# Optimization experiments

Measured on AMD Instinct MI355X. Metric: run time of the kernel, lower is better.

Reference implementation:

```python
import jax, jax.numpy as jnp
import numpy as np

S, B, IN, OUT = 32, 256, 1024, 1024

def setup_inputs() -> dict:
    key = jax.random.key(0)
    ks = jax.random.split(key, 7)
    return {
        "input": jax.random.normal(ks[0], (S, B, IN), dtype=jnp.float32),
        "weight_mu": jax.random.normal(ks[1], (OUT, IN), dtype=jnp.float32) * 0.1,
        "weight_rho": jax.random.normal(ks[2], (OUT, IN), dtype=jnp.float32) - 3.0,
        "bias_mu": jax.random.normal(ks[3], (OUT,), dtype=jnp.float32) * 0.1,
        "bias_rho": jax.random.normal(ks[4], (OUT,), dtype=jnp.float32) - 3.0,
        "eps_w": jax.random.normal(ks[5], (S, OUT, IN), dtype=jnp.float32),
        "eps_b": jax.random.normal(ks[6], (S, OUT), dtype=jnp.float32),
    }

def reference(input, weight_mu, weight_rho, bias_mu, bias_rho, eps_w, eps_b):
    # sigma = log(1 + exp(rho))  (softplus)
    weight_sigma = jax.nn.softplus(weight_rho)              # (out, in)
    bias_sigma = jax.nn.softplus(bias_rho)                  # (out,)
    # reparameterized samples: (S, out, in) and (S, out)
    weight = weight_mu[None, :, :] + weight_sigma[None, :, :] * eps_w
    bias = bias_mu[None, :] + bias_sigma[None, :] * eps_b
    # batch_linear: per-sample x @ W^T + b
    out = jnp.einsum('sbi,soi->sbo', input, weight) + bias[:, None, :]
    return out
```

## Files before the change

### kernel.cpp

```cpp
#include <hip/hip_runtime.h>
#include <hip/hip_bf16.h>

constexpr int kS   = 32;
constexpr int kB   = 256;
constexpr int kIN  = 1024;
constexpr int kOUT = 1024;
constexpr int BN   = 64;
constexpr int BK   = 32;
constexpr int NT   = kIN / BK;

typedef __bf16 v4bf __attribute__((ext_vector_type(4)));
typedef __bf16 v8bf __attribute__((ext_vector_type(8)));
typedef float  v4f  __attribute__((ext_vector_type(4)));

__device__ __forceinline__ float softplus_f(float x) {
    return fmaxf(x, 0.0f) + log1pf(expf(-fabsf(x)));
}
__device__ __forceinline__ unsigned int bfbits(float x) {
    __bf16 h = (__bf16)x;
    unsigned short u;
    __builtin_memcpy(&u, &h, 2);
    return (unsigned int)u;
}
__device__ __forceinline__ float asf(unsigned int u) {
    float f; __builtin_memcpy(&f, &u, 4); return f;
}

__global__ void sigma_pack(const float* __restrict__ mu, const float* __restrict__ rho,
                           uint4* __restrict__ ms) {
    int gid = blockIdx.x * blockDim.x + threadIdx.x;
    float4 m = reinterpret_cast<const float4*>(mu)[gid];
    float4 r = reinterpret_cast<const float4*>(rho)[gid];
    uint4 o;
    o.x = bfbits(m.x) | (bfbits(softplus_f(r.x)) << 16);
    o.y = bfbits(m.y) | (bfbits(softplus_f(r.y)) << 16);
    o.z = bfbits(m.z) | (bfbits(softplus_f(r.z)) << 16);
    o.w = bfbits(m.w) | (bfbits(softplus_f(r.w)) << 16);
    ms[gid] = o;
}

__global__ void xcast_kernel(const float* __restrict__ X, __bf16* __restrict__ Xb) {
    size_t i = ((size_t)blockIdx.x * blockDim.x + threadIdx.x) * 8;
    float4 a = *reinterpret_cast<const float4*>(X + i);
    float4 b = *reinterpret_cast<const float4*>(X + i + 4);
    v8bf r;
    r[0] = (__bf16)a.x; r[1] = (__bf16)a.y; r[2] = (__bf16)a.z; r[3] = (__bf16)a.w;
    r[4] = (__bf16)b.x; r[5] = (__bf16)b.y; r[6] = (__bf16)b.z; r[7] = (__bf16)b.w;
    *reinterpret_cast<v8bf*>(Xb + i) = r;
}

__global__ __launch_bounds__(256, 4) void wmat(
        const unsigned int* __restrict__ MS,
        const float* __restrict__ Ew,
        __bf16* __restrict__ Wp)
{
    const int bb  = blockIdx.x;
    const int s   = bb & 31;
    const int rr  = bb >> 5;
    const int ot  = rr >> 2;
    const int q   = rr & 3;
    const int tid = threadIdx.x;

    const float*        Eg = Ew + ((size_t)s * kOUT + ot * 64) * kIN;
    const unsigned int* Mg = MS + (size_t)(ot * 64) * kIN;
    char* Wt = (char*)(Wp + ((size_t)(s * 16 + ot) * NT) * 2048);

    #pragma unroll 4
    for (int i = tid; i < 16 * 256; i += 256) {
        int row = q * 16 + (i >> 8);
        int k   = (i & 255) * 4;
        float4 e = *reinterpret_cast<const float4*>(Eg + (size_t)row * kIN + k);
        uint4  p = *reinterpret_cast<const uint4*>(Mg + (size_t)row * kIN + k);
        v4bf w;
        w[0] = (__bf16)fmaf(asf(p.x & 0xffff0000u), e.x, asf(p.x << 16));
        w[1] = (__bf16)fmaf(asf(p.y & 0xffff0000u), e.y, asf(p.y << 16));
        w[2] = (__bf16)fmaf(asf(p.z & 0xffff0000u), e.z, asf(p.z << 16));
        w[3] = (__bf16)fmaf(asf(p.w & 0xffff0000u), e.w, asf(p.w << 16));
        int t    = k >> 5;
        int slot = ((k >> 3) & 3) ^ ((row >> 1) & 3);
        *reinterpret_cast<v4bf*>(Wt + t * 4096 + row * 64 + slot * 16 + (k & 7) * 2) = w;
    }
}

#define GLDS16(g, l) __builtin_amdgcn_global_load_lds(                      \
    (const __attribute__((address_space(1))) void*)(g),                     \
    (__attribute__((address_space(3))) void*)(l), 16, 0, 0)
#define GLDS4(g, l) __builtin_amdgcn_global_load_lds(                       \
    (const __attribute__((address_space(1))) void*)(g),                     \
    (__attribute__((address_space(3))) void*)(l), 4, 0, 0)

__global__ __launch_bounds__(512, 4) void dv_gemm(
        const __bf16* __restrict__ Xb,
        const __bf16* __restrict__ Wp,
        const float* __restrict__ Bmu,
        const float* __restrict__ Brho,
        const float* __restrict__ Eb,
        float* __restrict__ O)
{
    __shared__ __attribute__((aligned(16))) __bf16 Xs[3][kB * BK];
    __shared__ __attribute__((aligned(16))) __bf16 Ws[3][BN * BK];

    const int tid = threadIdx.x, bb = blockIdx.x;
    const int xcd = bb & 7;
    const int jj  = bb >> 3;
    const int s   = (xcd << 2) | (jj & 3);
    const int ot  = jj >> 2;
    const int o_base = ot * BN;

    const int lane = tid & 63, wv = tid >> 6;
    const int mwv = wv >> 1, nwv = wv & 1;
    const int lr = lane & 15, kg = lane >> 4;

    const __bf16* Xbase = Xb + (size_t)s * kB * kIN;
    const char*   Wbase = (const char*)(Wp + ((size_t)(s * 16 + ot) * NT) * 2048);

    const int xrow = wv * 32 + (lane >> 2);
    const int xq0  = ((lane & 3) - (xrow >> 2)) & 3;
    const int xq1  = ((lane & 3) - ((xrow + 16) >> 2)) & 3;

    auto STAGE = [&](int t, int bf) {
        GLDS16(Xbase + (size_t)xrow * kIN + t * BK + xq0 * 8,
               &Xs[bf][(wv * 32) * BK]);
        GLDS16(Xbase + (size_t)(xrow + 16) * kIN + t * BK + xq1 * 8,
               &Xs[bf][(wv * 32 + 16) * BK]);
        const char* wt = Wbase + t * 4096 + wv * 512;
        char*       wl = (char*)&Ws[bf][0] + wv * 512;
        GLDS4(wt + lane * 4,       wl);
        GLDS4(wt + 256 + lane * 4, wl + 256);
    };

    v4f acc[4][2] = {};

    STAGE(0, 0);
    STAGE(1, 1);

    for (int t = 0; t < NT; ++t) {
        const int bf = t % 3;

        if (t < NT - 1)
            asm volatile("s_waitcnt vmcnt(4) lgkmcnt(0)" ::: "memory");
        else
            asm volatile("s_waitcnt vmcnt(0) lgkmcnt(0)" ::: "memory");
        __builtin_amdgcn_s_barrier();

        if (t + 2 < NT) STAGE(t + 2, (t + 2) % 3);

        v8bf a[4];
        #pragma unroll
        for (int mf = 0; mf < 4; ++mf) {
            int row = mwv * 64 + mf * 16 + lr;
            int ql  = (kg + (row >> 2)) & 3;
            a[mf] = *reinterpret_cast<const v8bf*>(&Xs[bf][row * BK + ql * 8]);
        }
        v8bf b[2];
        #pragma unroll
        for (int nf = 0; nf < 2; ++nf) {
            int row  = nwv * 32 + nf * 16 + lr;
            int slot = kg ^ ((row >> 1) & 3);
            b[nf] = *reinterpret_cast<const v8bf*>(
                (const char*)&Ws[bf][0] + row * 64 + slot * 16);
        }

        #pragma unroll
        for (int mf = 0; mf < 4; ++mf)
            #pragma unroll
            for (int nf = 0; nf < 2; ++nf)
                acc[mf][nf] = __builtin_amdgcn_mfma_f32_16x16x32_bf16(
                    a[mf], b[nf], acc[mf][nf], 0, 0, 0);
    }

    float bias[2];
    #pragma unroll
    for (int nf = 0; nf < 2; ++nf) {
        int o = o_base + nwv * 32 + nf * 16 + lr;
        bias[nf] = fmaf(softplus_f(Brho[o]), Eb[(size_t)s * kOUT + o], Bmu[o]);
    }
    #pragma unroll
    for (int mf = 0; mf < 4; ++mf) {
        #pragma unroll
        for (int rr = 0; rr < 4; ++rr) {
            int mrow = mwv * 64 + mf * 16 + kg * 4 + rr;
            float* orow = O + ((size_t)s * kB + mrow) * kOUT + o_base + nwv * 32;
            #pragma unroll
            for (int nf = 0; nf < 2; ++nf)
                __builtin_nontemporal_store(acc[mf][nf][rr] + bias[nf],
                                            orow + nf * 16 + lr);
        }
    }
}

__global__ void dv_naive(const float* __restrict__ X, const float* __restrict__ Wmu,
                         const float* __restrict__ Wrho, const float* __restrict__ Bmu,
                         const float* __restrict__ Brho, const float* __restrict__ Ew,
                         const float* __restrict__ Eb, float* __restrict__ O) {
    size_t gid = (size_t)blockIdx.x * blockDim.x + threadIdx.x;
    int o = gid % kOUT;
    int b = (gid / kOUT) % kB;
    int s = gid / ((size_t)kOUT * kB);
    const float* x = X + ((size_t)s * kB + b) * kIN;
    const float* e = Ew + ((size_t)s * kOUT + o) * kIN;
    const float* wm = Wmu + (size_t)o * kIN;
    const float* wr = Wrho + (size_t)o * kIN;
    float acc = 0.f;
    for (int k = 0; k < kIN; ++k)
        acc += x[k] * fmaf(softplus_f(wr[k]), e[k], wm[k]);
    O[gid] = acc + fmaf(softplus_f(Brho[o]), Eb[(size_t)s * kOUT + o], Bmu[o]);
}

extern "C" void kernel_launch(void* const* d_in, const int* in_sizes, int n_in,
                              void* d_out, int out_size, void* d_ws, size_t ws_size,
                              hipStream_t stream) {
    const float* input = (const float*)d_in[0];
    const float* w_mu  = (const float*)d_in[1];
    const float* w_rho = (const float*)d_in[2];
    const float* b_mu  = (const float*)d_in[3];
    const float* b_rho = (const float*)d_in[4];
    const float* eps_w = (const float*)d_in[5];
    const float* eps_b = (const float*)d_in[6];
    float* out = (float*)d_out;

    const size_t ms_bytes  = (size_t)kOUT * kIN * 4;
    const size_t xbf_bytes = (size_t)kS * kB * kIN * sizeof(__bf16);
    const size_t wp_bytes  = (size_t)kS * kOUT * kIN * sizeof(__bf16);

    if (ws_size < ms_bytes + xbf_bytes + wp_bytes) {
        dv_naive<<<dim3((size_t)kS * kB * kOUT / 256), 256, 0, stream>>>(
            input, w_mu, w_rho, b_mu, b_rho, eps_w, eps_b, out);
        return;
    }

    unsigned int* ms = (unsigned int*)d_ws;
    __bf16* xbf = (__bf16*)((char*)d_ws + ms_bytes);
    __bf16* wp  = (__bf16*)((char*)d_ws + ms_bytes + xbf_bytes);

    sigma_pack<<<dim3((kOUT * kIN) / (256 * 4)), 256, 0, stream>>>(w_mu, w_rho, (uint4*)ms);
    xcast_kernel<<<dim3((size_t)kS * kB * kIN / (256 * 8)), 256, 0, stream>>>(input, xbf);
    wmat<<<dim3(2048), 256, 0, stream>>>(ms, eps_w, wp);
    dv_gemm<<<dim3(kS * (kOUT / BN)), 512, 0, stream>>>(xbf, wp, b_mu, b_rho, eps_b, out);
}
```

Before: 302.1 us.

## Fuse weight sampling into GEMM by staging eps_w and packed mu/sigma in LDS

Removes the separate wmat kernel and its bf16 weight buffer. The GEMM now streams fp32 eps_w chunks and packed mu/sigma rows into double-buffered LDS, then builds the bf16 B fragments in registers with an FMA just before the MFMAs. The output tile shrinks from 64 to 32 columns, with a new multi-stream waitcnt schedule. This avoids writing and re-reading the materialised weight tensor in HBM. The cost is that X is read twice as often, and the larger LDS footprint likely leaves only one block per CU, which weakens latency hiding.

```diff
diff --git a/kernel.cpp b/kernel.cpp
--- a/kernel.cpp
+++ b/kernel.cpp
@@ -5,11 +5,11 @@
 constexpr int kB   = 256;
 constexpr int kIN  = 1024;
 constexpr int kOUT = 1024;
-constexpr int BN   = 64;
+constexpr int BN   = 32;
 constexpr int BK   = 32;
+constexpr int CK   = 256;
 constexpr int NT   = kIN / BK;
 
-typedef __bf16 v4bf __attribute__((ext_vector_type(4)));
 typedef __bf16 v8bf __attribute__((ext_vector_type(8)));
 typedef float  v4f  __attribute__((ext_vector_type(4)));
 
@@ -49,56 +49,22 @@
     *reinterpret_cast<v8bf*>(Xb + i) = r;
 }
 
-__global__ __launch_bounds__(256, 4) void wmat(
-        const unsigned int* __restrict__ MS,
-        const float* __restrict__ Ew,
-        __bf16* __restrict__ Wp)
-{
-    const int bb  = blockIdx.x;
-    const int s   = bb & 31;
-    const int rr  = bb >> 5;
-    const int ot  = rr >> 2;
-    const int q   = rr & 3;
-    const int tid = threadIdx.x;
-
-    const float*        Eg = Ew + ((size_t)s * kOUT + ot * 64) * kIN;
-    const unsigned int* Mg = MS + (size_t)(ot * 64) * kIN;
-    char* Wt = (char*)(Wp + ((size_t)(s * 16 + ot) * NT) * 2048);
-
-    #pragma unroll 4
-    for (int i = tid; i < 16 * 256; i += 256) {
-        int row = q * 16 + (i >> 8);
-        int k   = (i & 255) * 4;
-        float4 e = *reinterpret_cast<const float4*>(Eg + (size_t)row * kIN + k);
-        uint4  p = *reinterpret_cast<const uint4*>(Mg + (size_t)row * kIN + k);
-        v4bf w;
-        w[0] = (__bf16)fmaf(asf(p.x & 0xffff0000u), e.x, asf(p.x << 16));
-        w[1] = (__bf16)fmaf(asf(p.y & 0xffff0000u), e.y, asf(p.y << 16));
-        w[2] = (__bf16)fmaf(asf(p.z & 0xffff0000u), e.z, asf(p.z << 16));
-        w[3] = (__bf16)fmaf(asf(p.w & 0xffff0000u), e.w, asf(p.w << 16));
-        int t    = k >> 5;
-        int slot = ((k >> 3) & 3) ^ ((row >> 1) & 3);
-        *reinterpret_cast<v4bf*>(Wt + t * 4096 + row * 64 + slot * 16 + (k & 7) * 2) = w;
-    }
-}
-
 #define GLDS16(g, l) __builtin_amdgcn_global_load_lds(                      \
     (const __attribute__((address_space(1))) void*)(g),                     \
     (__attribute__((address_space(3))) void*)(l), 16, 0, 0)
-#define GLDS4(g, l) __builtin_amdgcn_global_load_lds(                       \
-    (const __attribute__((address_space(1))) void*)(g),                     \
-    (__attribute__((address_space(3))) void*)(l), 4, 0, 0)
-
-__global__ __launch_bounds__(512, 4) void dv_gemm(
+
+__global__ __launch_bounds__(512, 2) void dv_main(
         const __bf16* __restrict__ Xb,
-        const __bf16* __restrict__ Wp,
+        const unsigned int* __restrict__ MS,
+        const float* __restrict__ Ew,
         const float* __restrict__ Bmu,
         const float* __restrict__ Brho,
         const float* __restrict__ Eb,
         float* __restrict__ O)
 {
-    __shared__ __attribute__((aligned(16))) __bf16 Xs[3][kB * BK];
-    __shared__ __attribute__((aligned(16))) __bf16 Ws[3][BN * BK];
+    __shared__ __attribute__((aligned(16))) float        Ep[2][BN * CK];
+    __shared__ __attribute__((aligned(16))) unsigned int Mp[2][BN * (CK/2)];
+    __shared__ __attribute__((aligned(16))) __bf16       Xs[3][kB * BK];
 
     const int tid = threadIdx.x, bb = blockIdx.x;
     const int xcd = bb & 7;
@@ -108,61 +74,96 @@
     const int o_base = ot * BN;
 
     const int lane = tid & 63, wv = tid >> 6;
-    const int mwv = wv >> 1, nwv = wv & 1;
     const int lr = lane & 15, kg = lane >> 4;
 
     const __bf16* Xbase = Xb + (size_t)s * kB * kIN;
-    const char*   Wbase = (const char*)(Wp + ((size_t)(s * 16 + ot) * NT) * 2048);
-
     const int xrow = wv * 32 + (lane >> 2);
     const int xq0  = ((lane & 3) - (xrow >> 2)) & 3;
     const int xq1  = ((lane & 3) - ((xrow + 16) >> 2)) & 3;
 
-    auto STAGE = [&](int t, int bf) {
+    auto STAGE_X = [&](int t, int bf) {
         GLDS16(Xbase + (size_t)xrow * kIN + t * BK + xq0 * 8,
                &Xs[bf][(wv * 32) * BK]);
         GLDS16(Xbase + (size_t)(xrow + 16) * kIN + t * BK + xq1 * 8,
                &Xs[bf][(wv * 32 + 16) * BK]);
-        const char* wt = Wbase + t * 4096 + wv * 512;
-        char*       wl = (char*)&Ws[bf][0] + wv * 512;
-        GLDS4(wt + lane * 4,       wl);
-        GLDS4(wt + 256 + lane * 4, wl + 256);
     };
-
-    v4f acc[4][2] = {};
-
-    STAGE(0, 0);
-    STAGE(1, 1);
-
-    for (int t = 0; t < NT; ++t) {
-        const int bf = t % 3;
-
-        if (t < NT - 1)
+    auto STAGE_E = [&](int c, int bf) {
+        #pragma unroll
+        for (int j = 0; j < 4; ++j) {
+            int r = wv * 4 + j;
+            GLDS16(Ew + ((size_t)s * kOUT + o_base + r) * kIN + c * CK
+                       + ((lane ^ (r & 7)) << 2),
+                   (char*)&Ep[bf][0] + r * 1024);
+        }
+    };
+    auto STAGE_M = [&](int sub, int bf) {
+        #pragma unroll
+        for (int j = 0; j < 2; ++j) {
+            int r0 = j * 16 + wv * 2;
+            int r  = r0 + (lane >> 5);
+            GLDS16(MS + (size_t)(o_base + r) * kIN + sub * 128
+                      + (((lane & 31) ^ (r & 7)) << 2),
+                   (char*)&Mp[bf][0] + r0 * 512);
+        }
+    };
+
+    v4f acc[2][2] = {};
+
+    STAGE_E(0, 0);
+    STAGE_M(0, 0);
+    STAGE_X(0, 0);
+    STAGE_X(1, 1);
+
+    #pragma unroll
+    for (int T = 0; T < NT; ++T) {
+        if (T == 1 || T == 9 || T == 17)
+            asm volatile("s_waitcnt vmcnt(8) lgkmcnt(0)" ::: "memory");
+        else if (T == 5 || T == 13 || T == 21 || T == 25)
             asm volatile("s_waitcnt vmcnt(4) lgkmcnt(0)" ::: "memory");
+        else if (T == 31)
+            asm volatile("s_waitcnt vmcnt(0) lgkmcnt(0)" ::: "memory");
         else
-            asm volatile("s_waitcnt vmcnt(0) lgkmcnt(0)" ::: "memory");
+            asm volatile("s_waitcnt vmcnt(2) lgkmcnt(0)" ::: "memory");
         __builtin_amdgcn_s_barrier();
 
-        if (t + 2 < NT) STAGE(t + 2, (t + 2) % 3);
-
-        v8bf a[4];
-        #pragma unroll
-        for (int mf = 0; mf < 4; ++mf) {
-            int row = mwv * 64 + mf * 16 + lr;
+        if ((T & 7) == 0 && T < 24) STAGE_E(T / 8 + 1, (T / 8 + 1) & 1);
+        if ((T & 3) == 0 && T < 28) STAGE_M(T / 4 + 1, (T / 4 + 1) & 1);
+        if (T < 30)                 STAGE_X(T + 2, (T + 2) % 3);
+
+        const int bf = T % 3;
+        v8bf a[2];
+        #pragma unroll
+        for (int mf = 0; mf < 2; ++mf) {
+            int row = wv * 32 + mf * 16 + lr;
             int ql  = (kg + (row >> 2)) & 3;
             a[mf] = *reinterpret_cast<const v8bf*>(&Xs[bf][row * BK + ql * 8]);
         }
+
+        const char* eb = (const char*)&Ep[(T >> 3) & 1][0];
+        const char* mb = (const char*)&Mp[(T >> 2) & 1][0];
         v8bf b[2];
         #pragma unroll
         for (int nf = 0; nf < 2; ++nf) {
-            int row  = nwv * 32 + nf * 16 + lr;
-            int slot = kg ^ ((row >> 1) & 3);
-            b[nf] = *reinterpret_cast<const v8bf*>(
-                (const char*)&Ws[bf][0] + row * 64 + slot * 16);
-        }
-
-        #pragma unroll
-        for (int mf = 0; mf < 4; ++mf)
+            int r  = nf * 16 + lr;
+            int sw = r & 7;
+            int g0  = (T & 7) * 8 + kg * 2;
+            int g0m = (T & 3) * 8 + kg * 2;
+            float4 e0 = *reinterpret_cast<const float4*>(eb + r * 1024 + ((g0 ^ sw) << 4));
+            float4 e1 = *reinterpret_cast<const float4*>(eb + r * 1024 + (((g0 + 1) ^ sw) << 4));
+            uint4  p0 = *reinterpret_cast<const uint4*>(mb + r * 512 + ((g0m ^ sw) << 4));
+            uint4  p1 = *reinterpret_cast<const uint4*>(mb + r * 512 + (((g0m + 1) ^ sw) << 4));
+            b[nf][0] = (__bf16)fmaf(asf(p0.x & 0xffff0000u), e0.x, asf(p0.x << 16));
+            b[nf][1] = (__bf16)fmaf(asf(p0.y & 0xffff0000u), e0.y, asf(p0.y << 16));
+            b[nf][2] = (__bf16)fmaf(asf(p0.z & 0xffff0000u), e0.z, asf(p0.z << 16));
+            b[nf][3] = (__bf16)fmaf(asf(p0.w & 0xffff0000u), e0.w, asf(p0.w << 16));
+            b[nf][4] = (__bf16)fmaf(asf(p1.x & 0xffff0000u), e1.x, asf(p1.x << 16));
+            b[nf][5] = (__bf16)fmaf(asf(p1.y & 0xffff0000u), e1.y, asf(p1.y << 16));
+            b[nf][6] = (__bf16)fmaf(asf(p1.z & 0xffff0000u), e1.z, asf(p1.z << 16));
+            b[nf][7] = (__bf16)fmaf(asf(p1.w & 0xffff0000u), e1.w, asf(p1.w << 16));
+        }
+
+        #pragma unroll
+        for (int mf = 0; mf < 2; ++mf)
             #pragma unroll
             for (int nf = 0; nf < 2; ++nf)
                 acc[mf][nf] = __builtin_amdgcn_mfma_f32_16x16x32_bf16(
@@ -172,15 +173,15 @@
     float bias[2];
     #pragma unroll
     for (int nf = 0; nf < 2; ++nf) {
-        int o = o_base + nwv * 32 + nf * 16 + lr;
+        int o = o_base + nf * 16 + lr;
         bias[nf] = fmaf(softplus_f(Brho[o]), Eb[(size_t)s * kOUT + o], Bmu[o]);
     }
     #pragma unroll
-    for (int mf = 0; mf < 4; ++mf) {
+    for (int mf = 0; mf < 2; ++mf) {
         #pragma unroll
         for (int rr = 0; rr < 4; ++rr) {
-            int mrow = mwv * 64 + mf * 16 + kg * 4 + rr;
-            float* orow = O + ((size_t)s * kB + mrow) * kOUT + o_base + nwv * 32;
+            int mrow = wv * 32 + mf * 16 + kg * 4 + rr;
+            float* orow = O + ((size_t)s * kB + mrow) * kOUT + o_base;
             #pragma unroll
             for (int nf = 0; nf < 2; ++nf)
                 __builtin_nontemporal_store(acc[mf][nf][rr] + bias[nf],
@@ -221,9 +222,8 @@
 
     const size_t ms_bytes  = (size_t)kOUT * kIN * 4;
     const size_t xbf_bytes = (size_t)kS * kB * kIN * sizeof(__bf16);
-    const size_t wp_bytes  = (size_t)kS * kOUT * kIN * sizeof(__bf16);
-
-    if (ws_size < ms_bytes + xbf_bytes + wp_bytes) {
+
+    if (ws_size < ms_bytes + xbf_bytes) {
         dv_naive<<<dim3((size_t)kS * kB * kOUT / 256), 256, 0, stream>>>(
             input, w_mu, w_rho, b_mu, b_rho, eps_w, eps_b, out);
         return;
@@ -231,10 +231,10 @@
 
     unsigned int* ms = (unsigned int*)d_ws;
     __bf16* xbf = (__bf16*)((char*)d_ws + ms_bytes);
-    __bf16* wp  = (__bf16*)((char*)d_ws + ms_bytes + xbf_bytes);
 
     sigma_pack<<<dim3((kOUT * kIN) / (256 * 4)), 256, 0, stream>>>(w_mu, w_rho, (uint4*)ms);
     xcast_kernel<<<dim3((size_t)kS * kB * kIN / (256 * 8)), 256, 0, stream>>>(input, xbf);
-    wmat<<<dim3(2048), 256, 0, stream>>>(ms, eps_w, wp);
-    dv_gemm<<<dim3(kS * (kOUT / BN)), 512, 0, stream>>>(xbf, wp, b_mu, b_rho, eps_b, out);
-}
+
+    dim3 grid(kS * (kOUT / BN));
+    dv_main<<<grid, 512, 0, stream>>>(xbf, ms, eps_w, b_mu, b_rho, eps_b, out);
+}
```

Result: no change. 306.9 us (+1.6%).
